# Kernel optimization log

Measured on AMD Instinct MI355X. Metric: run time of the kernel, lower is better.

Reference implementation:

```python
import jax, jax.numpy as jnp
import numpy as np

RES = 64

TRI_TABLE = jnp.array([
    [-1,-1,-1,-1,-1,-1],[1,0,2,-1,-1,-1],[4,0,3,-1,-1,-1],[1,4,2,1,3,4],
    [3,1,5,-1,-1,-1],[2,3,0,2,5,3],[1,4,0,1,5,4],[4,2,5,-1,-1,-1],
    [4,5,2,-1,-1,-1],[4,1,0,4,5,1],[3,2,0,3,5,2],[1,3,5,-1,-1,-1],
    [4,1,2,4,3,1],[3,0,4,-1,-1,-1],[2,0,1,-1,-1,-1],[-1,-1,-1,-1,-1,-1]], dtype=jnp.int32)
NUM_TRI = jnp.array([0,1,1,2,1,2,2,1,1,2,2,1,2,1,1,0], dtype=jnp.int32)
BASE_EDGES = jnp.array([0,1,0,2,0,3,1,2,1,3,2,3], dtype=jnp.int32)


def _make_tet_grid(res):
    # Kuhn 6-tet decomposition of each cube of a (res+1)^3 grid.
    n = res + 1
    ii, jj, kk = np.meshgrid(np.arange(n), np.arange(n), np.arange(n), indexing='ij')
    verts = (np.stack([ii, jj, kk], -1).reshape(-1, 3).astype(np.float32)) / res
    def vid(i, j, k):
        return (i * n + j) * n + k
    i, j, k = np.meshgrid(np.arange(res), np.arange(res), np.arange(res), indexing='ij')
    i, j, k = i.ravel(), j.ravel(), k.ravel()
    c = [vid(i + (b & 1), j + ((b >> 1) & 1), k + ((b >> 2) & 1)) for b in range(8)]
    kuhn = [(0,1,3,7),(0,3,2,7),(0,2,6,7),(0,6,4,7),(0,4,5,7),(0,5,1,7)]
    tets = np.stack([np.stack([c[a], c[b], c[d], c[e]], -1) for (a, b, d, e) in kuhn], 1)
    return verts, tets.reshape(-1, 4).astype(np.int64)


def setup_inputs() -> dict:
    key = jax.random.key(0)
    verts, tets = _make_tet_grid(RES)
    level = jax.random.normal(key, (verts.shape[0], 1), dtype=jnp.float32)
    return {"level": level, "pos": jnp.asarray(verts), "tet": jnp.asarray(tets), "threshold": 0}


def reference(level, pos, tet, threshold):
    sdf = level - threshold                    # [N,1]
    occ = sdf[:, 0] > 0                        # [N]
    occ_fx4 = occ[tet]                         # [F,4]
    occ_sum = occ_fx4.sum(-1)
    valid = (occ_sum > 0) & (occ_sum < 4)
    vt = tet[valid]                            # [Fv,4]
    occ_valid = occ_fx4[valid]                 # [Fv,4]

    edges = jnp.sort(vt[:, BASE_EDGES].reshape(-1, 2), axis=1)   # [Fv*6,2]
    unique_edges, idx_map = jnp.unique(edges, axis=0, return_inverse=True)
    idx_map = idx_map.reshape(-1)
    mask_edges = occ[unique_edges].sum(-1) == 1                  # crossing edges
    mapping = jnp.where(mask_edges, jnp.cumsum(mask_edges) - 1, -1)
    idx_map = mapping[idx_map].reshape(-1, 6)                    # [Fv,6]
    interp_v = unique_edges[mask_edges]                          # [M,2]

    p = pos[interp_v]                                            # [M,2,3]
    s = sdf[interp_v][..., 0] * jnp.array([1.0, -1.0], dtype=sdf.dtype)  # [M,2]
    w = s[:, ::-1] / s.sum(1, keepdims=True)                     # flip / denom
    verts_out = (p * w[..., None]).sum(1)                        # [M,3]

    v_id = 2 ** jnp.arange(4, dtype=jnp.int32)
    tetindex = (occ_valid.astype(jnp.int32) * v_id).sum(-1)      # [Fv]
    num_tri = NUM_TRI[tetindex]
    m1, m2 = num_tri == 1, num_tri == 2
    f1 = jnp.take_along_axis(idx_map[m1], TRI_TABLE[tetindex[m1]][:, :3], axis=1).reshape(-1, 3)
    f2 = jnp.take_along_axis(idx_map[m2], TRI_TABLE[tetindex[m2]][:, :6], axis=1).reshape(-1, 3)
    faces = jnp.concatenate([f1, f2], axis=0)
    return verts_out, faces
```

## Files before the change

kernel.cpp:

```cpp
#include <hip/hip_runtime.h>


#define RESX 64
#define NV   65
#define NV2  4225
#define NVERT 274625
#define NCUBE 262144
#define BLOCK 256
#define NGE 4225
#define NGC 4096
#define NB1I 1024
#define NBND 129
#define NBLK1 1057
#define CBLK 1024
#define NFB 33
#define STAGE 9216
#define M21 0x1fffffu
#define NTRI_PACK 0x16696994u

__constant__ int c_tri[16][6] = {
    {-1,-1,-1,-1,-1,-1},{1,0,2,-1,-1,-1},{4,0,3,-1,-1,-1},{1,4,2,1,3,4},
    {3,1,5,-1,-1,-1},{2,3,0,2,5,3},{1,4,0,1,5,4},{4,2,5,-1,-1,-1},
    {4,5,2,-1,-1,-1},{4,1,0,4,5,1},{3,2,0,3,5,2},{1,3,5,-1,-1,-1},
    {4,1,2,4,3,1},{3,0,4,-1,-1,-1},{2,0,1,-1,-1,-1},{-1,-1,-1,-1,-1,-1}};
__constant__ int c_kuhn[6][4] = {{0,1,3,7},{0,3,2,7},{0,2,6,7},{0,6,4,7},{0,4,5,7},{0,5,1,7}};
__constant__ int c_off8[8] = {0,4225,65,4290,1,4226,66,4291};
__constant__ int c_loc[6][6] = {
    {0,0,0,1,1,3},{0,0,0,2,3,2},{0,0,0,2,2,6},
    {0,0,0,4,6,4},{0,0,0,4,4,5},{0,0,0,1,5,1}};
__constant__ int c_dir[6][6] = {
    {3,5,6,1,2,0},{5,1,6,3,0,4},{1,2,6,0,4,3},
    {2,0,6,1,3,5},{0,4,6,3,5,1},{4,3,6,0,1,2}};

typedef unsigned long long u64;

__device__ __forceinline__ unsigned block_scan_excl(unsigned val, unsigned* lds,
                                                    unsigned& block_total) {
    int tid = threadIdx.x, lane = tid & 63, w = tid >> 6;
    unsigned x = val;
#pragma unroll
    for (int off = 1; off < 64; off <<= 1) {
        unsigned y = (unsigned)__shfl_up((int)x, off, 64);
        if (lane >= off) x += y;
    }
    if (lane == 63) lds[w] = x;
    __syncthreads();
    if (tid == 0) {
        unsigned s = 0;
#pragma unroll
        for (int i = 0; i < 4; i++) { unsigned t = lds[i]; lds[i + 4] = s; s += t; }
        lds[8] = s;
    }
    __syncthreads();
    block_total = lds[8];
    return x - val + lds[4 + w];
}

__global__ void __launch_bounds__(256)
pass1(const float* __restrict__ level, const float* __restrict__ thrp,
      unsigned char* __restrict__ flagsArr, unsigned short* __restrict__ locEx,
      unsigned* __restrict__ bsE, unsigned* __restrict__ bsC) {
    int tid = threadIdx.x, lane = tid & 63, w = tid >> 6;
    int bid = blockIdx.x;
    float thr = thrp[0];
    unsigned fl = 0, fl65 = 0, c1 = 0, c2 = 0;
    int base, grp, cgrp = -1;

    if (bid < NB1I) {
        int ci = bid >> 4, cj = ((bid & 15) << 2) + w;
        grp = ci * NV + cj;
        base = grp * NV;
        int v = base + lane;
        float r0  = level[v]        - thr;
        float rY  = level[v + 65]   - thr;
        float rX  = level[v + 4225] - thr;
        float rXY = level[v + 4290] - thr;
        float t0 = 0.f, tY = 0.f, tX = 0.f, tXY = 0.f;
        if (lane == 63) {
            t0  = level[base + 64]   - thr;
            tY  = level[base + 129]  - thr;
            tX  = level[base + 4289] - thr;
            tXY = level[base + 4354] - thr;
        }
        float a4 = __shfl_down(r0, 1, 64);  if (lane == 63) a4 = t0;
        float a6 = __shfl_down(rY, 1, 64);  if (lane == 63) a6 = tY;
        float a5 = __shfl_down(rX, 1, 64);  if (lane == 63) a5 = tX;
        float a7 = __shfl_down(rXY, 1, 64); if (lane == 63) a7 = tXY;
        bool s0 = r0 > 0.f;
        fl = s0 ? 0x80u : 0u;
        if ((a4  > 0.f) != s0) fl |= 1u;
        if ((rY  > 0.f) != s0) fl |= 2u;
        if ((a6  > 0.f) != s0) fl |= 4u;
        if ((rX  > 0.f) != s0) fl |= 8u;
        if ((a5  > 0.f) != s0) fl |= 16u;
        if ((rXY > 0.f) != s0) fl |= 32u;
        if ((a7  > 0.f) != s0) fl |= 64u;
        unsigned occ8 = (r0  > 0.f ?   1u : 0u) | (rX  > 0.f ?   2u : 0u)
                      | (rY  > 0.f ?   4u : 0u) | (rXY > 0.f ?   8u : 0u)
                      | (a4  > 0.f ?  16u : 0u) | (a5  > 0.f ?  32u : 0u)
                      | (a6  > 0.f ?  64u : 0u) | (a7  > 0.f ? 128u : 0u);
#pragma unroll
        for (int t = 0; t < 6; t++) {
            int cfg = ((occ8 >> c_kuhn[t][0]) & 1) | (((occ8 >> c_kuhn[t][1]) & 1) << 1)
                    | (((occ8 >> c_kuhn[t][2]) & 1) << 2) | (((occ8 >> c_kuhn[t][3]) & 1) << 3);
            unsigned nt = (NTRI_PACK >> (cfg << 1)) & 3u;
            c1 += (nt == 1); c2 += (nt == 2);
        }
        if (lane == 63) {
            bool s65 = t0 > 0.f;
            fl65 = s65 ? 0x80u : 0u;
            if ((tY  > 0.f) != s65) fl65 |= 2u;
            if ((tX  > 0.f) != s65) fl65 |= 8u;
            if ((tXY > 0.f) != s65) fl65 |= 32u;
        }
        cgrp = (ci << 6) + cj;
    } else {
        int bw = (bid - NB1I) * 4 + w;
        if (bw >= NBND) return;
        if (bw < 64) {
            grp = bw * NV + 64;
            base = grp * NV;
            int v = base + lane;
            float r0 = level[v]        - thr;
            float rX = level[v + 4225] - thr;
            float t0 = 0.f, tX = 0.f;
            if (lane == 63) { t0 = level[base + 64] - thr; tX = level[base + 4289] - thr; }
            float a1 = __shfl_down(r0, 1, 64); if (lane == 63) a1 = t0;
            float a5 = __shfl_down(rX, 1, 64); if (lane == 63) a5 = tX;
            bool s0 = r0 > 0.f;
            fl = s0 ? 0x80u : 0u;
            if ((a1 > 0.f) != s0) fl |= 1u;
            if ((rX > 0.f) != s0) fl |= 8u;
            if ((a5 > 0.f) != s0) fl |= 16u;
            if (lane == 63) {
                bool s65 = t0 > 0.f;
                fl65 = s65 ? 0x80u : 0u;
                if ((tX > 0.f) != s65) fl65 |= 8u;
            }
        } else if (bw < 128) {
            int j = bw - 64;
            grp = 64 * NV + j;
            base = grp * NV;
            int v = base + lane;
            float r0 = level[v]      - thr;
            float rY = level[v + 65] - thr;
            float t0 = 0.f, tY = 0.f;
            if (lane == 63) { t0 = level[base + 64] - thr; tY = level[base + 129] - thr; }
            float a1 = __shfl_down(r0, 1, 64); if (lane == 63) a1 = t0;
            float a3 = __shfl_down(rY, 1, 64); if (lane == 63) a3 = tY;
            bool s0 = r0 > 0.f;
            fl = s0 ? 0x80u : 0u;
            if ((a1 > 0.f) != s0) fl |= 1u;
            if ((rY > 0.f) != s0) fl |= 2u;
            if ((a3 > 0.f) != s0) fl |= 4u;
            if (lane == 63) {
                bool s65 = t0 > 0.f;
                fl65 = s65 ? 0x80u : 0u;
                if ((tY > 0.f) != s65) fl65 |= 2u;
            }
        } else {
            grp = 64 * NV + 64;
            base = grp * NV;
            int v = base + lane;
            float r0 = level[v] - thr;
            float t0 = 0.f;
            if (lane == 63) t0 = level[base + 64] - thr;
            float a1 = __shfl_down(r0, 1, 64); if (lane == 63) a1 = t0;
            bool s0 = r0 > 0.f;
            fl = s0 ? 0x80u : 0u;
            if ((a1 > 0.f) != s0) fl |= 1u;
            if (lane == 63) fl65 = (t0 > 0.f) ? 0x80u : 0u;
        }
    }

    unsigned cnt65 = __popc(fl65 & 0x7fu);
    unsigned cnt = __popc(fl & 0x7fu);
    unsigned val = cnt | (c1 << 10) | (c2 << 20);
    unsigned x = val;
#pragma unroll
    for (int off = 1; off < 64; off <<= 1) {
        unsigned y = (unsigned)__shfl_up((int)x, off, 64);
        if (lane >= off) x += y;
    }
    int v = base + lane;
    flagsArr[v] = (unsigned char)fl;
    locEx[v] = (unsigned short)((x - val) & 0x3ffu);
    if (lane == 63) {
        unsigned totE64 = x & 0x3ffu;
        flagsArr[base + 64] = (unsigned char)fl65;
        locEx[base + 64] = (unsigned short)totE64;
        bsE[grp] = totE64 + cnt65;
        if (cgrp >= 0)
            bsC[cgrp] = ((x >> 10) & 0x3ffu) | (((x >> 20) & 0x3ffu) << 16);
    }
}

__global__ void __launch_bounds__(1024)
scanK(const unsigned* __restrict__ bsE, const unsigned* __restrict__ bsC,
      unsigned* __restrict__ preE, uint2* __restrict__ preC) {
    __shared__ unsigned lws[16];
    __shared__ u64 lwc[16];
    int tid = threadIdx.x, lane = tid & 63, w = tid >> 6;
    unsigned ev[5]; unsigned s = 0;
#pragma unroll
    for (int e = 0; e < 5; e++) {
        int idx = tid * 5 + e;
        unsigned a = (idx < NGE) ? bsE[idx] : 0u;
        ev[e] = a; s += a;
    }
    unsigned x = s;
#pragma unroll
    for (int off = 1; off < 64; off <<= 1) {
        unsigned y = (unsigned)__shfl_up((int)x, off, 64);
        if (lane >= off) x += y;
    }
    if (lane == 63) lws[w] = x;
    __syncthreads();
    if (tid == 0) {
        unsigned acc = 0;
#pragma unroll
        for (int i = 0; i < 16; i++) { unsigned t = lws[i]; lws[i] = acc; acc += t; }
    }
    __syncthreads();
    unsigned run = x - s + lws[w];
#pragma unroll
    for (int e = 0; e < 5; e++) {
        int idx = tid * 5 + e;
        if (idx <= NGE) preE[idx] = run;
        run += ev[e];
    }
    u64 cv[4]; u64 cs = 0;
#pragma unroll
    for (int e = 0; e < 4; e++) {
        int idx = tid * 4 + e;
        unsigned a = (idx < NGC) ? bsC[idx] : 0u;
        u64 p = (u64)(a & 0xffffu) | ((u64)(a >> 16) << 21);
        cv[e] = p; cs += p;
    }
    u64 cx = cs;
#pragma unroll
    for (int off = 1; off < 64; off <<= 1) {
        u64 y = __shfl_up(cx, off, 64);
        if (lane >= off) cx += y;
    }
    if (lane == 63) lwc[w] = cx;
    __syncthreads();
    if (tid == 0) {
        u64 acc = 0;
#pragma unroll
        for (int i = 0; i < 16; i++) { u64 t = lwc[i]; lwc[i] = acc; acc += t; }
    }
    __syncthreads();
    u64 crun = cx - cs + lwc[w];
#pragma unroll
    for (int e = 0; e < 4; e++) {
        int idx = tid * 4 + e;
        if (idx < NGC)
            preC[idx] = make_uint2((unsigned)(crun & M21), (unsigned)((crun >> 21) & M21));
        crun += cv[e];
    }
    if (tid == 1023)
        preC[NGC] = make_uint2((unsigned)(crun & M21), (unsigned)((crun >> 21) & M21));
}

__global__ void __launch_bounds__(256)
pass2(const float* __restrict__ level, const float* __restrict__ thrp,
      const unsigned char* __restrict__ flagsArr,
      const unsigned short* __restrict__ locEx,
      const unsigned* __restrict__ preE, const uint2* __restrict__ preC,
      float* __restrict__ out) {
    __shared__ unsigned lds[9];
    __shared__ unsigned pEw[10];
    __shared__ float stage[STAGE];
    int tid = threadIdx.x, bid = blockIdx.x;
    int gid = bid * BLOCK + tid;
    float thr = thrp[0];
    int ci = bid >> 4, cj0 = (bid & 15) << 2;
    int grpA = ci * NV + cj0;
    unsigned pE = preE[grpA];
    unsigned totE_blk = preE[grpA + 4] - pE;
    if (tid < 10) pEw[tid] = preE[(ci + tid / 5) * NV + cj0 + tid % 5];
    uint2 pc = preC[4 * bid];
    unsigned M = preE[NGE];
    unsigned C1 = preC[NGC].x;

    {
        int u = tid;
#pragma unroll
        for (int pass = 0; pass < 2; pass++) {
            if (pass == 1) { if (tid >= 4) break; u = 256 + tid; }
            int jr = (u >= 195) ? 3 : (u >= 130) ? 2 : (u >= 65) ? 1 : 0;
            int k = u - jr * 65;
            int vid = (grpA + jr) * NV + k;
            float lv[8];
#pragma unroll
            for (int b = 0; b < 8; b++) {
                int a = vid + c_off8[b];
                lv[b] = level[a < NVERT ? a : 0] - thr;
            }
            unsigned fl = flagsArr[vid];
            if (fl & 0x7fu) {
                unsigned slot = (preE[grpA + jr] - pE) + locEx[vid];
                float v0 = lv[0];
                const float inv = 1.f / 64.f;
                const int d2b[7] = {4, 2, 6, 1, 5, 3, 7};
                float fi = (float)ci, fj = (float)(cj0 + jr), fk = (float)k;
                float* o = &stage[3u * slot];
#pragma unroll
                for (int d = 0; d < 7; d++) {
                    if (fl & (1u << d)) {
                        const int b = d2b[d];
                        float w1 = v0 * __builtin_amdgcn_rcpf(v0 - lv[b]);
                        o[0] = (fi + (float)(b & 1) * w1) * inv;
                        o[1] = (fj + (float)((b >> 1) & 1) * w1) * inv;
                        o[2] = (fk + (float)((b >> 2) & 1) * w1) * inv;
                        o += 3;
                    }
                }
            }
        }
    }
    __syncthreads();
    {
        float* dst = out + 3u * pE;
        unsigned n = totE_blk * 3u;
        for (unsigned idx = tid; idx < n; idx += BLOCK)
            __builtin_nontemporal_store(stage[idx], &dst[idx]);
    }
    if (bid < NFB) {
        __syncthreads();
        int u = tid;
#pragma unroll
        for (int pass = 0; pass < 2; pass++) {
            if (pass == 1) { if (tid >= 4) break; u = 256 + tid; }
            int gsel = (u >= 195) ? 3 : (u >= 130) ? 2 : (u >= 65) ? 1 : 0;
            int k = u - gsel * 65;
            int bg = 4 * bid + gsel;
            if (bg < NBND) {
                int i, j;
                if (bg < 64) { i = bg; j = 64; }
                else         { i = 64; j = bg - 64; }
                int vid = (i * NV + j) * NV + k;
                float lv[8];
#pragma unroll
                for (int b = 0; b < 8; b++) {
                    int a = vid + c_off8[b];
                    lv[b] = level[a < NVERT ? a : 0] - thr;
                }
                unsigned fl = flagsArr[vid];
                if (fl & 0x7fu) {
                    unsigned slot = locEx[vid];
                    float v0 = lv[0];
                    const float inv = 1.f / 64.f;
                    const int d2b[7] = {4, 2, 6, 1, 5, 3, 7};
                    float fi = (float)i, fj = (float)j, fk = (float)k;
                    float* o = &stage[1365u * (unsigned)gsel + 3u * slot];
#pragma unroll
                    for (int d = 0; d < 7; d++) {
                        if (fl & (1u << d)) {
                            const int b = d2b[d];
                            float w1 = v0 * __builtin_amdgcn_rcpf(v0 - lv[b]);
                            o[0] = (fi + (float)(b & 1) * w1) * inv;
                            o[1] = (fj + (float)((b >> 1) & 1) * w1) * inv;
                            o[2] = (fk + (float)((b >> 2) & 1) * w1) * inv;
                            o += 3;
                        }
                    }
                }
            }
        }
        __syncthreads();
#pragma unroll
        for (int gsel = 0; gsel < 4; gsel++) {
            int bg = 4 * bid + gsel;
            if (bg >= NBND) break;
            int grp = (bg < 64) ? bg * NV + 64 : 64 * NV + (bg - 64);
            unsigned pg = preE[grp];
            unsigned n = (preE[grp + 1] - pg) * 3u;
            float* dst = out + 3u * pg;
            for (unsigned idx = tid; idx < n; idx += BLOCK)
                __builtin_nontemporal_store(stage[1365u * (unsigned)gsel + idx], &dst[idx]);
        }
    }
    __syncthreads();

    int ccj = (gid >> 6) & 63, cck = gid & 63;
    int cj_rel = ccj & 3;
    int basev = (ci * NV + ccj) * NV + cck;
    u64 f8 = 0ull;
#pragma unroll
    for (int b = 0; b < 8; b++)
        f8 |= (u64)flagsArr[basev + c_off8[b]] << (8 * b);
    unsigned occ8 = 0;
#pragma unroll
    for (int b = 0; b < 8; b++) occ8 |= (unsigned)((f8 >> (8 * b + 7)) & 1ull) << b;
    int cfgs[6];
    unsigned c1 = 0, c2 = 0;
#pragma unroll
    for (int t = 0; t < 6; t++) {
        int cfg = ((occ8 >> c_kuhn[t][0]) & 1) | (((occ8 >> c_kuhn[t][1]) & 1) << 1)
                | (((occ8 >> c_kuhn[t][2]) & 1) << 2) | (((occ8 >> c_kuhn[t][3]) & 1) << 3);
        cfgs[t] = cfg;
        unsigned nt = (NTRI_PACK >> (cfg << 1)) & 3u;
        c1 += (nt == 1); c2 += (nt == 2);
    }
    unsigned tot2;
    unsigned ex2 = block_scan_excl(c1 | (c2 << 16), lds, tot2);
    unsigned f1 = tot2 & 0xffffu;
    unsigned f2 = tot2 >> 16;
    unsigned l1c = ex2 & 0xffffu;
    unsigned l2c = ex2 >> 16;
    unsigned n1 = f1 * 3u;
#pragma unroll
    for (int t = 0; t < 6; t++) {
        int cfg = cfgs[t];
        unsigned nt = (NTRI_PACK >> (cfg << 1)) & 3u;
        if (nt == 0) continue;
        auto rank = [&](int e) -> float {
            int lc = c_loc[t][e];
            int dir = c_dir[t][e];
            int lo = basev + c_off8[lc];
            unsigned flb = (unsigned)((f8 >> (8 * lc)) & 0xffull);
            int widx = (lc & 1) * 5 + cj_rel + ((lc >> 1) & 1);
            return (float)(pEw[widx] + locEx[lo] + __popc(flb & ((1u << dir) - 1u)));
        };
        float ra = rank(c_tri[cfg][0]);
        float rb = rank(c_tri[cfg][1]);
        float rc = rank(c_tri[cfg][2]);
        if (nt == 1) {
            unsigned bfo = 3u * l1c;
            stage[bfo] = ra; stage[bfo + 1] = rb; stage[bfo + 2] = rc;
            l1c++;
        } else {
            float rd = rank(c_tri[cfg][4]);
            unsigned bfo = n1 + 6u * l2c;
            stage[bfo]     = ra; stage[bfo + 1] = rb; stage[bfo + 2] = rc;
            stage[bfo + 3] = ra; stage[bfo + 4] = rd; stage[bfo + 5] = rb;
            l2c++;
        }
    }
    __syncthreads();
    float* of = out + 3ull * M;
    float* o1 = of + 3u * pc.x;
    for (unsigned idx = tid; idx < n1; idx += BLOCK)
        __builtin_nontemporal_store(stage[idx], &o1[idx]);
    unsigned n2 = f2 * 6u;
    float* o2 = of + 3u * (C1 + 2u * pc.y);
    for (unsigned idx = tid; idx < n2; idx += BLOCK)
        __builtin_nontemporal_store(stage[n1 + idx], &o2[idx]);
}

extern "C" void kernel_launch(void* const* d_in, const int* in_sizes, int n_in,
                              void* d_out, int out_size, void* d_ws, size_t ws_size,
                              hipStream_t stream) {
    const float* level = (const float*)d_in[0];
    const float* thrp = (const float*)d_in[3];
    float* out = (float*)d_out;

    char* p = (char*)d_ws;
    unsigned char* flagsArr = (unsigned char*)p;
    p += (NVERT + 255) & ~255;
    unsigned short* locEx = (unsigned short*)p;
    p += ((sizeof(unsigned short) * NVERT) + 255) & ~255;
    unsigned* bsE = (unsigned*)p;
    p += ((sizeof(unsigned) * NGE) + 255) & ~255;
    unsigned* bsC = (unsigned*)p;
    p += ((sizeof(unsigned) * NGC) + 255) & ~255;
    unsigned* preE = (unsigned*)p;
    p += ((sizeof(unsigned) * (NGE + 1)) + 255) & ~255;
    uint2* preC = (uint2*)p;

    pass1<<<NBLK1, BLOCK, 0, stream>>>(level, thrp, flagsArr, locEx, bsE, bsC);
    scanK<<<1, 1024, 0, stream>>>(bsE, bsC, preE, preC);
    pass2<<<CBLK, BLOCK, 0, stream>>>(level, thrp, flagsArr, locEx, preE, preC, out);
}
```

Measured before the change: 112.5 us.

## Recompute vertex flags via wave shuffles, stage flags/ranks in LDS, split scan

In pass2, per-vertex crossing flags and local slots are now recomputed from level values using wave shuffles and a wave-level scan, replacing the per-vertex 8-neighbour level gathers and the flagsArr/locEx lookups. The flags and local ranks for the block's 10 rows are loaded once into shared memory, and the face phase reads from there instead of global memory. The scan kernel is split across two blocks so the edge and cube prefix sums run concurrently, and some preC/preE loads are deferred to the end of pass2. This cuts redundant global gathers at the cost of more LDS use and duplicated flag logic.

```diff
diff --git a/kernel.cpp b/kernel.cpp
--- a/kernel.cpp
+++ b/kernel.cpp
@@ -5,7 +5,6 @@
 #define NV   65
 #define NV2  4225
 #define NVERT 274625
-#define NCUBE 262144
 #define BLOCK 256
 #define NGE 4225
 #define NGC 4096
@@ -54,6 +53,39 @@
     __syncthreads();
     block_total = lds[8];
     return x - val + lds[4 + w];
+}
+
+__device__ __forceinline__ unsigned wave_excl(unsigned cnt, unsigned& incl) {
+    int lane = threadIdx.x & 63;
+    unsigned x = cnt;
+#pragma unroll
+    for (int off = 1; off < 64; off <<= 1) {
+        unsigned y = (unsigned)__shfl_up((int)x, off, 64);
+        if (lane >= off) x += y;
+    }
+    incl = x;
+    return x - cnt;
+}
+
+__device__ __forceinline__ void emit_vtx(unsigned fl, const float lv[8],
+                                         float fi, float fj, float fk,
+                                         unsigned slot, float* stage) {
+    if (!(fl & 0x7fu)) return;
+    float v0 = lv[0];
+    const float inv = 1.f / 64.f;
+    const int d2b[7] = {4, 2, 6, 1, 5, 3, 7};
+    float* o = &stage[3u * slot];
+#pragma unroll
+    for (int d = 0; d < 7; d++) {
+        if (fl & (1u << d)) {
+            const int b = d2b[d];
+            float w1 = v0 * __builtin_amdgcn_rcpf(v0 - lv[b]);
+            o[0] = (fi + (float)(b & 1) * w1) * inv;
+            o[1] = (fj + (float)((b >> 1) & 1) * w1) * inv;
+            o[2] = (fk + (float)((b >> 2) & 1) * w1) * inv;
+            o += 3;
+        }
+    }
 }
 
 __global__ void __launch_bounds__(256)
@@ -198,69 +230,72 @@
 __global__ void __launch_bounds__(1024)
 scanK(const unsigned* __restrict__ bsE, const unsigned* __restrict__ bsC,
       unsigned* __restrict__ preE, uint2* __restrict__ preC) {
-    __shared__ unsigned lws[16];
-    __shared__ u64 lwc[16];
     int tid = threadIdx.x, lane = tid & 63, w = tid >> 6;
-    unsigned ev[5]; unsigned s = 0;
-#pragma unroll
-    for (int e = 0; e < 5; e++) {
-        int idx = tid * 5 + e;
-        unsigned a = (idx < NGE) ? bsE[idx] : 0u;
-        ev[e] = a; s += a;
-    }
-    unsigned x = s;
-#pragma unroll
-    for (int off = 1; off < 64; off <<= 1) {
-        unsigned y = (unsigned)__shfl_up((int)x, off, 64);
-        if (lane >= off) x += y;
-    }
-    if (lane == 63) lws[w] = x;
-    __syncthreads();
-    if (tid == 0) {
-        unsigned acc = 0;
-#pragma unroll
-        for (int i = 0; i < 16; i++) { unsigned t = lws[i]; lws[i] = acc; acc += t; }
-    }
-    __syncthreads();
-    unsigned run = x - s + lws[w];
-#pragma unroll
-    for (int e = 0; e < 5; e++) {
-        int idx = tid * 5 + e;
-        if (idx <= NGE) preE[idx] = run;
-        run += ev[e];
-    }
-    u64 cv[4]; u64 cs = 0;
-#pragma unroll
-    for (int e = 0; e < 4; e++) {
-        int idx = tid * 4 + e;
-        unsigned a = (idx < NGC) ? bsC[idx] : 0u;
-        u64 p = (u64)(a & 0xffffu) | ((u64)(a >> 16) << 21);
-        cv[e] = p; cs += p;
-    }
-    u64 cx = cs;
-#pragma unroll
-    for (int off = 1; off < 64; off <<= 1) {
-        u64 y = __shfl_up(cx, off, 64);
-        if (lane >= off) cx += y;
-    }
-    if (lane == 63) lwc[w] = cx;
-    __syncthreads();
-    if (tid == 0) {
-        u64 acc = 0;
-#pragma unroll
-        for (int i = 0; i < 16; i++) { u64 t = lwc[i]; lwc[i] = acc; acc += t; }
-    }
-    __syncthreads();
-    u64 crun = cx - cs + lwc[w];
-#pragma unroll
-    for (int e = 0; e < 4; e++) {
-        int idx = tid * 4 + e;
-        if (idx < NGC)
-            preC[idx] = make_uint2((unsigned)(crun & M21), (unsigned)((crun >> 21) & M21));
-        crun += cv[e];
-    }
-    if (tid == 1023)
-        preC[NGC] = make_uint2((unsigned)(crun & M21), (unsigned)((crun >> 21) & M21));
+    if (blockIdx.x == 0) {
+        __shared__ unsigned lws[16];
+        unsigned ev[5]; unsigned s = 0;
+#pragma unroll
+        for (int e = 0; e < 5; e++) {
+            int idx = tid * 5 + e;
+            unsigned a = (idx < NGE) ? bsE[idx] : 0u;
+            ev[e] = a; s += a;
+        }
+        unsigned x = s;
+#pragma unroll
+        for (int off = 1; off < 64; off <<= 1) {
+            unsigned y = (unsigned)__shfl_up((int)x, off, 64);
+            if (lane >= off) x += y;
+        }
+        if (lane == 63) lws[w] = x;
+        __syncthreads();
+        if (tid == 0) {
+            unsigned acc = 0;
+#pragma unroll
+            for (int i = 0; i < 16; i++) { unsigned t = lws[i]; lws[i] = acc; acc += t; }
+        }
+        __syncthreads();
+        unsigned run = x - s + lws[w];
+#pragma unroll
+        for (int e = 0; e < 5; e++) {
+            int idx = tid * 5 + e;
+            if (idx <= NGE) preE[idx] = run;
+            run += ev[e];
+        }
+    } else {
+        __shared__ u64 lwc[16];
+        u64 cv[4]; u64 cs = 0;
+#pragma unroll
+        for (int e = 0; e < 4; e++) {
+            int idx = tid * 4 + e;
+            unsigned a = (idx < NGC) ? bsC[idx] : 0u;
+            u64 p = (u64)(a & 0xffffu) | ((u64)(a >> 16) << 21);
+            cv[e] = p; cs += p;
+        }
+        u64 cx = cs;
+#pragma unroll
+        for (int off = 1; off < 64; off <<= 1) {
+            u64 y = __shfl_up(cx, off, 64);
+            if (lane >= off) cx += y;
+        }
+        if (lane == 63) lwc[w] = cx;
+        __syncthreads();
+        if (tid == 0) {
+            u64 acc = 0;
+#pragma unroll
+            for (int i = 0; i < 16; i++) { u64 t = lwc[i]; lwc[i] = acc; acc += t; }
+        }
+        __syncthreads();
+        u64 crun = cx - cs + lwc[w];
+#pragma unroll
+        for (int e = 0; e < 4; e++) {
+            int idx = tid * 4 + e;
+            if (idx < NGC)
+                preC[idx] = make_uint2((unsigned)(crun & M21), (unsigned)((crun >> 21) & M21));
+            crun += cv[e];
+        }
+        if (tid == 1023)
+            preC[NGC] = make_uint2((unsigned)(crun & M21), (unsigned)((crun >> 21) & M21));
+    }
 }
 
 __global__ void __launch_bounds__(256)
@@ -271,53 +306,68 @@
       float* __restrict__ out) {
     __shared__ unsigned lds[9];
     __shared__ unsigned pEw[10];
+    __shared__ unsigned short rankW[650];
+    __shared__ unsigned char flagsW[656];
     __shared__ float stage[STAGE];
-    int tid = threadIdx.x, bid = blockIdx.x;
-    int gid = bid * BLOCK + tid;
+    int tid = threadIdx.x, bid = blockIdx.x, lane = tid & 63, w = tid >> 6;
     float thr = thrp[0];
     int ci = bid >> 4, cj0 = (bid & 15) << 2;
+    int ccj = cj0 + w;
     int grpA = ci * NV + cj0;
+    int grp = grpA + w;
     unsigned pE = preE[grpA];
     unsigned totE_blk = preE[grpA + 4] - pE;
     if (tid < 10) pEw[tid] = preE[(ci + tid / 5) * NV + cj0 + tid % 5];
-    uint2 pc = preC[4 * bid];
-    unsigned M = preE[NGE];
-    unsigned C1 = preC[NGC].x;
+    for (int idx = tid; idx < 650; idx += BLOCK) {
+        int wrow = idx / 65;
+        int kk = idx - wrow * 65;
+        int di = (wrow >= 5) ? 1 : 0;
+        int vid = ((ci + di) * NV + cj0 + wrow - 5 * di) * NV + kk;
+        rankW[idx] = locEx[vid];
+        flagsW[idx] = flagsArr[vid];
+    }
 
     {
-        int u = tid;
-#pragma unroll
-        for (int pass = 0; pass < 2; pass++) {
-            if (pass == 1) { if (tid >= 4) break; u = 256 + tid; }
-            int jr = (u >= 195) ? 3 : (u >= 130) ? 2 : (u >= 65) ? 1 : 0;
-            int k = u - jr * 65;
-            int vid = (grpA + jr) * NV + k;
-            float lv[8];
-#pragma unroll
-            for (int b = 0; b < 8; b++) {
-                int a = vid + c_off8[b];
-                lv[b] = level[a < NVERT ? a : 0] - thr;
-            }
-            unsigned fl = flagsArr[vid];
-            if (fl & 0x7fu) {
-                unsigned slot = (preE[grpA + jr] - pE) + locEx[vid];
-                float v0 = lv[0];
-                const float inv = 1.f / 64.f;
-                const int d2b[7] = {4, 2, 6, 1, 5, 3, 7};
-                float fi = (float)ci, fj = (float)(cj0 + jr), fk = (float)k;
-                float* o = &stage[3u * slot];
-#pragma unroll
-                for (int d = 0; d < 7; d++) {
-                    if (fl & (1u << d)) {
-                        const int b = d2b[d];
-                        float w1 = v0 * __builtin_amdgcn_rcpf(v0 - lv[b]);
-                        o[0] = (fi + (float)(b & 1) * w1) * inv;
-                        o[1] = (fj + (float)((b >> 1) & 1) * w1) * inv;
-                        o[2] = (fk + (float)((b >> 2) & 1) * w1) * inv;
-                        o += 3;
-                    }
-                }
-            }
+        int vbase = grp * NV;
+        int v = vbase + lane;
+        float r0  = level[v]        - thr;
+        float rY  = level[v + 65]   - thr;
+        float rX  = level[v + 4225] - thr;
+        float rXY = level[v + 4290] - thr;
+        float t0 = 0.f, tY = 0.f, tX = 0.f, tXY = 0.f;
+        if (lane == 63) {
+            t0  = level[vbase + 64]   - thr;
+            tY  = level[vbase + 129]  - thr;
+            tX  = level[vbase + 4289] - thr;
+            tXY = level[vbase + 4354] - thr;
+        }
+        float a4 = __shfl_down(r0, 1, 64);  if (lane == 63) a4 = t0;
+        float a6 = __shfl_down(rY, 1, 64);  if (lane == 63) a6 = tY;
+        float a5 = __shfl_down(rX, 1, 64);  if (lane == 63) a5 = tX;
+        float a7 = __shfl_down(rXY, 1, 64); if (lane == 63) a7 = tXY;
+        bool s0 = r0 > 0.f;
+        unsigned fl = s0 ? 0x80u : 0u;
+        if ((a4  > 0.f) != s0) fl |= 1u;
+        if ((rY  > 0.f) != s0) fl |= 2u;
+        if ((a6  > 0.f) != s0) fl |= 4u;
+        if ((rX  > 0.f) != s0) fl |= 8u;
+        if ((a5  > 0.f) != s0) fl |= 16u;
+        if ((rXY > 0.f) != s0) fl |= 32u;
+        if ((a7  > 0.f) != s0) fl |= 64u;
+        unsigned cnt = __popc(fl & 0x7fu);
+        unsigned incl, wex;
+        wex = wave_excl(cnt, incl);
+        unsigned slotRow = preE[grp] - pE;
+        float lv[8] = {r0, rX, rY, rXY, a4, a5, a6, a7};
+        emit_vtx(fl, lv, (float)ci, (float)ccj, (float)lane, slotRow + wex, stage);
+        if (lane == 63) {
+            bool s65 = t0 > 0.f;
+            unsigned fl65 = s65 ? 0x80u : 0u;
+            if ((tY  > 0.f) != s65) fl65 |= 2u;
+            if ((tX  > 0.f) != s65) fl65 |= 8u;
+            if ((tXY > 0.f) != s65) fl65 |= 32u;
+            float lv65[8] = {t0, tX, tY, tXY, 0.f, 0.f, 0.f, 0.f};
+            emit_vtx(fl65, lv65, (float)ci, (float)ccj, 64.f, slotRow + incl, stage);
         }
     }
     __syncthreads();
@@ -327,56 +377,62 @@
         for (unsigned idx = tid; idx < n; idx += BLOCK)
             __builtin_nontemporal_store(stage[idx], &dst[idx]);
     }
+
     if (bid < NFB) {
         __syncthreads();
-        int u = tid;
-#pragma unroll
-        for (int pass = 0; pass < 2; pass++) {
-            if (pass == 1) { if (tid >= 4) break; u = 256 + tid; }
-            int gsel = (u >= 195) ? 3 : (u >= 130) ? 2 : (u >= 65) ? 1 : 0;
-            int k = u - gsel * 65;
-            int bg = 4 * bid + gsel;
-            if (bg < NBND) {
-                int i, j;
-                if (bg < 64) { i = bg; j = 64; }
-                else         { i = 64; j = bg - 64; }
-                int vid = (i * NV + j) * NV + k;
-                float lv[8];
-#pragma unroll
-                for (int b = 0; b < 8; b++) {
-                    int a = vid + c_off8[b];
-                    lv[b] = level[a < NVERT ? a : 0] - thr;
-                }
-                unsigned fl = flagsArr[vid];
-                if (fl & 0x7fu) {
-                    unsigned slot = locEx[vid];
-                    float v0 = lv[0];
-                    const float inv = 1.f / 64.f;
-                    const int d2b[7] = {4, 2, 6, 1, 5, 3, 7};
-                    float fi = (float)i, fj = (float)j, fk = (float)k;
-                    float* o = &stage[1365u * (unsigned)gsel + 3u * slot];
-#pragma unroll
-                    for (int d = 0; d < 7; d++) {
-                        if (fl & (1u << d)) {
-                            const int b = d2b[d];
-                            float w1 = v0 * __builtin_amdgcn_rcpf(v0 - lv[b]);
-                            o[0] = (fi + (float)(b & 1) * w1) * inv;
-                            o[1] = (fj + (float)((b >> 1) & 1) * w1) * inv;
-                            o[2] = (fk + (float)((b >> 2) & 1) * w1) * inv;
-                            o += 3;
-                        }
-                    }
-                }
+        int bg = 4 * bid + w;
+        if (bg < NBND) {
+            int i, j;
+            if (bg < 64)       { i = bg; j = 64; }
+            else if (bg < 128) { i = 64; j = bg - 64; }
+            else               { i = 64; j = 64; }
+            int vbase = (i * NV + j) * NV;
+            int v = vbase + lane;
+            float r0 = level[v] - thr;
+            float t0 = (lane == 63) ? level[vbase + 64] - thr : 0.f;
+            float a1 = __shfl_down(r0, 1, 64); if (lane == 63) a1 = t0;
+            bool s0 = r0 > 0.f;
+            unsigned fl = s0 ? 0x80u : 0u;
+            if ((a1 > 0.f) != s0) fl |= 1u;
+            bool s65 = t0 > 0.f;
+            unsigned fl65 = s65 ? 0x80u : 0u;
+            float lv[8] = {r0, 0.f, 0.f, 0.f, a1, 0.f, 0.f, 0.f};
+            float lv65[8] = {t0, 0.f, 0.f, 0.f, 0.f, 0.f, 0.f, 0.f};
+            if (bg < 64) {
+                float rX = level[v + 4225] - thr;
+                float tX = (lane == 63) ? level[vbase + 4289] - thr : 0.f;
+                float a5 = __shfl_down(rX, 1, 64); if (lane == 63) a5 = tX;
+                if ((rX > 0.f) != s0) fl |= 8u;
+                if ((a5 > 0.f) != s0) fl |= 16u;
+                lv[1] = rX; lv[5] = a5;
+                if ((tX > 0.f) != s65) fl65 |= 8u;
+                lv65[1] = tX;
+            } else if (bg < 128) {
+                float rY = level[v + 65] - thr;
+                float tY = (lane == 63) ? level[vbase + 129] - thr : 0.f;
+                float a3 = __shfl_down(rY, 1, 64); if (lane == 63) a3 = tY;
+                if ((rY > 0.f) != s0) fl |= 2u;
+                if ((a3 > 0.f) != s0) fl |= 4u;
+                lv[2] = rY; lv[6] = a3;
+                if ((tY > 0.f) != s65) fl65 |= 2u;
+                lv65[2] = tY;
             }
+            unsigned cnt = __popc(fl & 0x7fu);
+            unsigned incl, wex;
+            wex = wave_excl(cnt, incl);
+            float* st = stage + 1365u * (unsigned)w;
+            emit_vtx(fl, lv, (float)i, (float)j, (float)lane, wex, st);
+            if (lane == 63)
+                emit_vtx(fl65, lv65, (float)i, (float)j, 64.f, incl, st);
         }
         __syncthreads();
 #pragma unroll
         for (int gsel = 0; gsel < 4; gsel++) {
-            int bg = 4 * bid + gsel;
-            if (bg >= NBND) break;
-            int grp = (bg < 64) ? bg * NV + 64 : 64 * NV + (bg - 64);
-            unsigned pg = preE[grp];
-            unsigned n = (preE[grp + 1] - pg) * 3u;
+            int bgf = 4 * bid + gsel;
+            if (bgf >= NBND) break;
+            int grpB = (bgf < 64) ? bgf * NV + 64 : 64 * NV + (bgf - 64);
+            unsigned pg = preE[grpB];
+            unsigned n = (preE[grpB + 1] - pg) * 3u;
             float* dst = out + 3u * pg;
             for (unsigned idx = tid; idx < n; idx += BLOCK)
                 __builtin_nontemporal_store(stage[1365u * (unsigned)gsel + idx], &dst[idx]);
@@ -384,13 +440,13 @@
     }
     __syncthreads();
 
-    int ccj = (gid >> 6) & 63, cck = gid & 63;
-    int cj_rel = ccj & 3;
-    int basev = (ci * NV + ccj) * NV + cck;
+    int kk = lane;
     u64 f8 = 0ull;
 #pragma unroll
-    for (int b = 0; b < 8; b++)
-        f8 |= (u64)flagsArr[basev + c_off8[b]] << (8 * b);
+    for (int b = 0; b < 8; b++) {
+        int widx = 5 * (b & 1) + w + ((b >> 1) & 1);
+        f8 |= (u64)flagsW[widx * 65 + kk + ((b >> 2) & 1)] << (8 * b);
+    }
     unsigned occ8 = 0;
 #pragma unroll
     for (int b = 0; b < 8; b++) occ8 |= (unsigned)((f8 >> (8 * b + 7)) & 1ull) << b;
@@ -419,10 +475,10 @@
         auto rank = [&](int e) -> float {
             int lc = c_loc[t][e];
             int dir = c_dir[t][e];
-            int lo = basev + c_off8[lc];
+            int widx = 5 * (lc & 1) + w + ((lc >> 1) & 1);
+            int lidx = widx * 65 + kk + ((lc >> 2) & 1);
             unsigned flb = (unsigned)((f8 >> (8 * lc)) & 0xffull);
-            int widx = (lc & 1) * 5 + cj_rel + ((lc >> 1) & 1);
-            return (float)(pEw[widx] + locEx[lo] + __popc(flb & ((1u << dir) - 1u)));
+            return (float)(pEw[widx] + rankW[lidx] + __popc(flb & ((1u << dir) - 1u)));
         };
         float ra = rank(c_tri[cfg][0]);
         float rb = rank(c_tri[cfg][1]);
@@ -440,6 +496,9 @@
         }
     }
     __syncthreads();
+    unsigned M = preE[NGE];
+    unsigned C1 = preC[NGC].x;
+    uint2 pc = preC[4 * bid];
     float* of = out + 3ull * M;
     float* o1 = of + 3u * pc.x;
     for (unsigned idx = tid; idx < n1; idx += BLOCK)
@@ -471,6 +530,6 @@
     uint2* preC = (uint2*)p;
 
     pass1<<<NBLK1, BLOCK, 0, stream>>>(level, thrp, flagsArr, locEx, bsE, bsC);
-    scanK<<<1, 1024, 0, stream>>>(bsE, bsC, preE, preC);
+    scanK<<<2, 1024, 0, stream>>>(bsE, bsC, preE, preC);
     pass2<<<CBLK, BLOCK, 0, stream>>>(level, thrp, flagsArr, locEx, preE, preC, out);
 }
```

Result: faster. 106.3 us (-5.5%).
